# Kernel tuning notes

Measured on AMD Instinct MI355X. Metric: run time of the kernel, lower is better.

The kernel has to match this reference:

```python
import jax, jax.numpy as jnp
import numpy as np

B, D, TOPC = 8, 1024, 256
CIN, DOWN, BR, NR, G = 64, 128, 2, 8, 8
GC = DOWN // G
H = W = 64
LN_EPS = 1e-5


def _ln(x, g, b):
    mu = x.mean(-1, keepdims=True)
    var = ((x - mu) ** 2).mean(-1, keepdims=True)
    return (x - mu) * jax.lax.rsqrt(var + LN_EPS) * g + b


def _gelu(x):
    return jax.nn.gelu(x, approximate=False)


def _sample_topleft(I, IX, IY, IT, x, y):
    # x, y: [B, N] continuous coords; returns [B, CIN, N]
    x = x[:, None, :]
    y = y[:, None, :]
    X = jnp.ceil(x).astype(jnp.int32)
    Y = jnp.ceil(y).astype(jnp.int32)
    z = jnp.zeros_like(X)
    dx = X - x
    dy = Y - y
    b = jnp.arange(B)[:, None, None]
    c = jnp.arange(CIN)[None, :, None]
    wx1 = 0.5 * dx ** 2
    wx2 = dx - wx1
    wy1 = 0.5 * dy ** 2
    wy2 = dy - wy1
    s_a = IT[b, c, X, Y]
    s_e1 = (wy1 * (IX[b, c, X, Y - 1] - 0.5 * I[b, c, X, Y - 1] - 0.5 * I[b, c, z, Y - 1])
            + wy2 * (IX[b, c, X, Y] - 0.5 * I[b, c, X, Y] - 0.5 * I[b, c, z, Y]))
    s_e2 = (wx1 * (IY[b, c, X - 1, Y] - 0.5 * I[b, c, X - 1, Y] - 0.5 * I[b, c, X - 1, z])
            + wx2 * (IY[b, c, X, Y] - 0.5 * I[b, c, X, Y] - 0.5 * I[b, c, X, z]))
    s_c = (wx1 * wy1 * I[b, c, X - 1, Y - 1] + wx2 * wy1 * I[b, c, X, Y - 1]
           + wx1 * wy2 * I[b, c, X - 1, Y] + wx2 * wy2 * I[b, c, X, Y])
    return s_a - s_e1 - s_e2 + s_c


def setup_inputs() -> dict:
    key = jax.random.key(0)
    ks = jax.random.split(key, 20)
    s = 0.02
    return {
        "x": jax.random.normal(ks[0], (B, D, TOPC), jnp.float32),
        "I": jax.random.normal(ks[1], (B, CIN, H, W), jnp.float32),
        "IX": jax.random.normal(ks[2], (B, CIN, H, W), jnp.float32),
        "IY": jax.random.normal(ks[3], (B, CIN, H, W), jnp.float32),
        "IT": jax.random.normal(ks[4], (B, CIN, H, W), jnp.float32),
        "w_idx": jax.random.normal(ks[5], (BR * NR * 4, TOPC), jnp.float32) * s,
        "b_idx": jnp.zeros((BR * NR * 4,), jnp.float32),
        "w_proj": jax.random.normal(ks[6], (DOWN, CIN), jnp.float32) * s,
        "b_proj": jnp.zeros((DOWN,), jnp.float32),
        "w_mask": jax.random.normal(ks[7], (BR * NR * G, TOPC), jnp.float32) * s,
        "b_mask": jnp.zeros((BR * NR * G,), jnp.float32),
        "g1": jnp.ones((DOWN,), jnp.float32),
        "beta1": jnp.zeros((DOWN,), jnp.float32),
        "w_mlp1": jax.random.normal(ks[8], (4 * DOWN, DOWN), jnp.float32) * s,
        "b_mlp1": jnp.zeros((4 * DOWN,), jnp.float32),
        "w_mlp2": jax.random.normal(ks[9], (DOWN, 4 * DOWN), jnp.float32) * s,
        "b_mlp2": jnp.zeros((DOWN,), jnp.float32),
        "g2": jnp.ones((DOWN,), jnp.float32),
        "beta2": jnp.zeros((DOWN,), jnp.float32),
    }


def reference(x, I, IX, IY, IT, w_idx, b_idx, w_proj, b_proj, w_mask, b_mask,
              g1, beta1, w_mlp1, b_mlp1, w_mlp2, b_mlp2, g2, beta2):
    # rect prediction
    p = x @ w_idx.T + b_idx                       # [B, D, BR*NR*4]
    fac = jnp.array([H - 1, W - 1, H - 1, W - 1], jnp.float32)
    p = jax.nn.sigmoid(p.reshape(B, D, BR, NR, 4)) * fac
    p = p.reshape(B, D * BR * NR, 4)
    x1, y1, x2, y2 = p[:, :, 0], p[:, :, 1], p[:, :, 2], p[:, :, 3]
    S = (_sample_topleft(I, IX, IY, IT, x2, y2)
         - _sample_topleft(I, IX, IY, IT, x1, y2)
         - _sample_topleft(I, IX, IY, IT, x2, y1)
         + _sample_topleft(I, IX, IY, IT, x1, y1))  # [B, CIN, N]
    S = S.reshape(B, CIN, D, BR, NR).transpose(0, 2, 3, 4, 1)  # [B, D, BR, NR, CIN]
    rects = _gelu(S @ w_proj.T + b_proj)           # [B, D, BR, NR, DOWN]
    mask = (x @ w_mask.T + b_mask).reshape(B, D * BR, NR, G, 1)
    mask = jax.nn.softmax(mask, axis=2)
    rects = rects.reshape(B, D * BR, NR, G, GC)
    out = (mask * rects).sum(2).reshape(B, D * BR, DOWN)
    out = _ln(out, g1, beta1)
    shortcut = out
    out = _gelu(out @ w_mlp1.T + b_mlp1) @ w_mlp2.T + b_mlp2
    return _ln(out, g2, beta2) + shortcut
```

## Files before the change

kernel.cpp:

```cpp
#include <hip/hip_runtime.h>
#include <hip/hip_bf16.h>
#include <hip/hip_fp16.h>
#include <math.h>

#define BB   8
#define DD   1024

typedef short bh8 __attribute__((ext_vector_type(8)));
typedef float f32x4 __attribute__((ext_vector_type(4)));
typedef _Float16 h2f __attribute__((ext_vector_type(2)));

__device__ __forceinline__ ushort f2bf(float f) {
    uint u = __builtin_bit_cast(uint, f);
    u += 0x7fffu + ((u >> 16) & 1u);
    return (ushort)(u >> 16);
}
__device__ __forceinline__ float asf(uint u)  { return __builtin_bit_cast(float, u); }
__device__ __forceinline__ float bflo(uint u) { return __builtin_bit_cast(float, u << 16); }
__device__ __forceinline__ float bfhi(uint u) { return __builtin_bit_cast(float, u & 0xffff0000u); }
__device__ __forceinline__ uint  pkh(float a, float b) {
    return __builtin_bit_cast(uint, __builtin_amdgcn_cvt_pkrtz(a, b));
}
__device__ __forceinline__ h2f ash2f(uint u) { return __builtin_bit_cast(h2f, u); }

#if __has_builtin(__builtin_amdgcn_fdot2)
__device__ __forceinline__ float fdot2h(h2f a, h2f b, float c) {
    return __builtin_amdgcn_fdot2(a, b, c, false);
}
#else
__device__ __forceinline__ float fdot2h(h2f a, h2f b, float c) {
    return fmaf((float)a.x, (float)b.x, fmaf((float)a.y, (float)b.y, c));
}
#endif

__device__ __forceinline__ uint cvtpk_bf16(float a, float b) {
    uint r;
    asm("v_cvt_pk_bf16_f32 %0, %1, %2" : "=v"(r) : "v"(a), "v"(b));
    return r;
}
__device__ __forceinline__ ushort cvt1_bf16(float a) {
    uint r;
    asm("v_cvt_pk_bf16_f32 %0, %1, %2" : "=v"(r) : "v"(a), "v"(a));
    return (ushort)r;
}

__device__ __forceinline__ float gelu_fast(float x) {
    float x2 = x * x;
#if __has_builtin(__builtin_amdgcn_exp2f)
    float e = __builtin_amdgcn_exp2f(x * fmaf(x2, -0.20588652f, -2.3022082f));
#else
    float e = __expf(-(1.5957691216f * x + 0.14270963f * x * x2));
#endif
    return x * __builtin_amdgcn_rcpf(1.0f + e);
}
__device__ __forceinline__ float sig63(float v) {
    return 63.0f * __builtin_amdgcn_rcpf(1.0f + __expf(-v));
}

__global__ __launch_bounds__(256) void kT_pack(
    const float* __restrict__ w_idx, const float* __restrict__ w_mask,
    const float* __restrict__ w_proj, const float* __restrict__ w1,
    const float* __restrict__ w2,
    ushort* __restrict__ catPh, ushort* __restrict__ catPm,
    ushort* __restrict__ catPl,
    ushort* __restrict__ w_projP, ushort* __restrict__ w1P,
    ushort* __restrict__ w2P)
{
    int bid = blockIdx.x, t = threadIdx.x;
    if (bid < 24) {
        int gid = bid * 256 + t;
        int l = gid & 63, ks = (gid >> 6) & 7, nt = gid >> 9;
        int n = nt * 16 + (l & 15);
        int kbase = ks * 32 + ((l >> 4) << 3);
        const float* src = (n < 64) ? (w_idx + (size_t)n * 256)
                                    : (w_mask + (size_t)(n - 64) * 256);
        ushort* dh = catPh + (size_t)gid * 8;
        ushort* dm = catPm + (size_t)gid * 8;
        ushort* dl = catPl + (size_t)gid * 8;
        #pragma unroll
        for (int j = 0; j < 8; ++j) {
            float v = src[kbase + j];
            ushort h = f2bf(v);
            float hf = __builtin_bit_cast(float, (uint)h << 16);
            float r1 = v - hf;
            ushort m = f2bf(r1); float mf = __builtin_bit_cast(float, (uint)m << 16);
            ushort lo = f2bf(r1 - mf);
            dh[j] = h; dm[j] = m; dl[j] = lo;
        }
    } else if (bid < 28) {
        int g = (bid - 24) * 256 + t;
        int nt = g >> 7, ks = (g >> 6) & 1, l = g & 63;
        int n = nt * 16 + (l & 15), k0 = ks * 32 + (l >> 4) * 8;
        ushort* dst = w_projP + (size_t)g * 8;
        #pragma unroll
        for (int j = 0; j < 8; ++j) dst[j] = f2bf(w_proj[n * 64 + k0 + j]);
    } else if (bid < 60) {
        int g = (bid - 28) * 256 + t;
        int nt = g >> 8, ks = (g >> 6) & 3, l = g & 63;
        int n = nt * 16 + (l & 15), k0 = ks * 32 + (l >> 4) * 8;
        ushort* dst = w1P + (size_t)g * 8;
        #pragma unroll
        for (int j = 0; j < 8; ++j) dst[j] = f2bf(w1[n * 128 + k0 + j]);
    } else {
        int g = (bid - 60) * 256 + t;
        int nt = g >> 10, ks = (g >> 6) & 15, l = g & 63;
        int n = nt * 16 + (l & 15), k0 = ks * 32 + (l >> 4) * 8;
        ushort* dst = w2P + (size_t)g * 8;
        #pragma unroll
        for (int j = 0; j < 8; ++j) dst[j] = f2bf(w2[n * 512 + k0 + j]);
    }
}

__global__ __launch_bounds__(256) void k01(
    const float* __restrict__ x,
    const ushort* __restrict__ catPh, const ushort* __restrict__ catPm,
    const ushort* __restrict__ catPl,
    const float* __restrict__ b_idx, const float* __restrict__ b_mask,
    float* __restrict__ maskw, float* __restrict__ coords,
    const float* __restrict__ I, const float* __restrict__ IX,
    const float* __restrict__ IY, const float* __restrict__ IT,
    uint4* __restrict__ T1, ushort* __restrict__ T2)
{
    __shared__ __align__(16) float sf[6528];
    int t = threadIdx.x;
    int bid = blockIdx.x;

    if (bid >= 2048) {
        float* sOut = sf;
        size_t rowbase = (size_t)(bid - 2048) * 16;
        int w = t >> 6, l = t & 63;

        f32x4 acc[3];
        acc[0] = (f32x4){0.f,0.f,0.f,0.f};
        acc[1] = (f32x4){0.f,0.f,0.f,0.f};
        acc[2] = (f32x4){0.f,0.f,0.f,0.f};
        const float* xr = x + (rowbase + (size_t)(l & 15)) * 256 + ((l >> 4) << 3);

        #pragma unroll
        for (int half = 0; half < 2; ++half) {
            bh8 Ah[4], Am[4], Al[4];
            #pragma unroll
            for (int k4 = 0; k4 < 4; ++k4) {
                int ks = half * 4 + k4;
                float4 v0 = *(const float4*)(xr + ks * 32);
                float4 v1 = *(const float4*)(xr + ks * 32 + 4);
                uint4 uh, um, ul;
                uh.x = cvtpk_bf16(v0.x, v0.y);
                uh.y = cvtpk_bf16(v0.z, v0.w);
                uh.z = cvtpk_bf16(v1.x, v1.y);
                uh.w = cvtpk_bf16(v1.z, v1.w);
                float r0a = v0.x - bflo(uh.x), r0b = v0.y - bfhi(uh.x);
                float r0c = v0.z - bflo(uh.y), r0d = v0.w - bfhi(uh.y);
                float r1a = v1.x - bflo(uh.z), r1b = v1.y - bfhi(uh.z);
                float r1c = v1.z - bflo(uh.w), r1d = v1.w - bfhi(uh.w);
                um.x = cvtpk_bf16(r0a, r0b);
                um.y = cvtpk_bf16(r0c, r0d);
                um.z = cvtpk_bf16(r1a, r1b);
                um.w = cvtpk_bf16(r1c, r1d);
                ul.x = cvtpk_bf16(r0a - bflo(um.x), r0b - bfhi(um.x));
                ul.y = cvtpk_bf16(r0c - bflo(um.y), r0d - bfhi(um.y));
                ul.z = cvtpk_bf16(r1a - bflo(um.z), r1b - bfhi(um.z));
                ul.w = cvtpk_bf16(r1c - bflo(um.w), r1d - bfhi(um.w));
                Ah[k4] = __builtin_bit_cast(bh8, uh);
                Am[k4] = __builtin_bit_cast(bh8, um);
                Al[k4] = __builtin_bit_cast(bh8, ul);
            }
            #pragma unroll
            for (int ntl = 0; ntl < 3; ++ntl) {
                int nt = w * 3 + ntl;
                #pragma unroll
                for (int k4 = 0; k4 < 4; ++k4) {
                    int ks = half * 4 + k4;
                    size_t fo = ((size_t)(nt * 8 + ks) * 64 + l) * 8;
                    bh8 bh = *(const bh8*)(catPh + fo);
                    bh8 bm = *(const bh8*)(catPm + fo);
                    bh8 bl = *(const bh8*)(catPl + fo);
                    acc[ntl] = __builtin_amdgcn_mfma_f32_16x16x32_bf16(Ah[k4], bh, acc[ntl], 0, 0, 0);
                    acc[ntl] = __builtin_amdgcn_mfma_f32_16x16x32_bf16(Ah[k4], bm, acc[ntl], 0, 0, 0);
                    acc[ntl] = __builtin_amdgcn_mfma_f32_16x16x32_bf16(Am[k4], bh, acc[ntl], 0, 0, 0);
                    acc[ntl] = __builtin_amdgcn_mfma_f32_16x16x32_bf16(Ah[k4], bl, acc[ntl], 0, 0, 0);
                    acc[ntl] = __builtin_amdgcn_mfma_f32_16x16x32_bf16(Al[k4], bh, acc[ntl], 0, 0, 0);
                    acc[ntl] = __builtin_amdgcn_mfma_f32_16x16x32_bf16(Am[k4], bm, acc[ntl], 0, 0, 0);
                }
            }
        }
        {
            int r0 = (l >> 4) * 4, cbase = w * 48 + (l & 15);
            #pragma unroll
            for (int ntl = 0; ntl < 3; ++ntl)
                #pragma unroll
                for (int reg = 0; reg < 4; ++reg)
                    sOut[(r0 + reg) * 193 + cbase + ntl * 16] = acc[ntl][reg];
        }
        __syncthreads();

        {
            int row = t >> 4, u = t & 15, br = u >> 3, nr = u & 7;
            const float* so = sOut + row * 193;
            int c0 = br * 32 + nr * 4;
            float4 co;
            co.x = sig63(so[c0 + 0] + b_idx[c0 + 0]);
            co.y = sig63(so[c0 + 1] + b_idx[c0 + 1]);
            co.z = sig63(so[c0 + 2] + b_idx[c0 + 2]);
            co.w = sig63(so[c0 + 3] + b_idx[c0 + 3]);
            *(float4*)(coords + (((rowbase + row) * 16) + (size_t)u) * 4) = co;
        }
        {
            int row = t >> 4, br = (t >> 3) & 1, g = t & 7;
            const float* so = sOut + row * 193 + 64;
            float lg[8];
            float mx = -1e30f;
            #pragma unroll
            for (int nr = 0; nr < 8; ++nr) {
                int idx = br * 64 + nr * 8 + g;
                lg[nr] = so[idx] + b_mask[idx];
                mx = fmaxf(mx, lg[nr]);
            }
            float s = 0.f;
            #pragma unroll
            for (int nr = 0; nr < 8; ++nr) { lg[nr] = __expf(lg[nr] - mx); s += lg[nr]; }
            float inv = __builtin_amdgcn_rcpf(s);
            #pragma unroll
            for (int nr = 0; nr < 8; ++nr)
                maskw[(rowbase + row) * 128 + br * 64 + nr * 8 + g] = lg[nr] * inv;
        }
    } else {
        int chunk = bid & 3, h = (bid >> 2) & 63, b = bid >> 8;
        int hp = h > 0 ? h - 1 : 0;
        int cb = chunk * 16;
        size_t inb  = (size_t)b * 262144 + (size_t)h  * 64;
        size_t inbp = (size_t)b * 262144 + (size_t)hp * 64;

        {
            int c = t >> 4, w4 = (t & 15) << 2;
            size_t o = (size_t)(cb + c) * 4096 + w4;
            int so = c * 68 + w4;
            *(float4*)(sf + 0 * 1088 + so) = *(const float4*)(I  + inb  + o);
            *(float4*)(sf + 1 * 1088 + so) = *(const float4*)(I  + inbp + o);
            *(float4*)(sf + 2 * 1088 + so) = *(const float4*)(IX + inb  + o);
            *(float4*)(sf + 3 * 1088 + so) = *(const float4*)(IY + inb  + o);
            *(float4*)(sf + 4 * 1088 + so) = *(const float4*)(IY + inbp + o);
            *(float4*)(sf + 5 * 1088 + so) = *(const float4*)(IT + inb  + o);
        }
        __syncthreads();

        #pragma unroll
        for (int i = 0; i < 4; ++i) {
            int idx = i * 256 + t; int w = idx >> 4, c = idx & 15;
            int wm = w > 0 ? w - 1 : 0;
            int rb = c * 68;
            float I00 = sf[rb + w],        I0m = sf[rb + wm];
            float Im0 = sf[1088 + rb + w], Imm = sf[1088 + rb + wm];
            float E1  = sf[2176 + rb + w]  - 0.5f * I00;
            float E1m = sf[2176 + rb + wm] - 0.5f * I0m;
            float E2  = sf[3264 + rb + w]  - 0.5f * I00;
            float E2m = sf[4352 + rb + w]  - 0.5f * Im0;
            float v0 = sf[5440 + rb + w];
            float v1 = -E1;
            float v2 = 0.5f * (E1 - E1m);
            float v3 = -E2;
            float v4 = 0.5f * (E2 - E2m);
            float v5 = I00;
            float v6 = 0.5f * (I0m - I00);
            float v7 = 0.5f * (Im0 - I00);
            float v8 = 0.25f * ((Imm - I0m) - (Im0 - I00));
            size_t pt = (((size_t)b * 4096) + (size_t)h * 64 + w) * 64 + (cb + c);
            uint4 o4;
            o4.x = pkh(v0, v1);
            o4.y = pkh(v2, v3);
            o4.z = pkh(v4, v5);
            o4.w = pkh(v6, v7);
            T1[pt] = o4;
            T2[pt] = (ushort)(pkh(v8, 0.f) & 0xffffu);
        }
    }
}

__global__ __launch_bounds__(256) void k2_rects(
    const uint4* __restrict__ T1, const ushort* __restrict__ T2,
    const float* __restrict__ coords,
    const ushort* __restrict__ w_projP, const float* __restrict__ b_proj,
    const float* __restrict__ maskw, const float* __restrict__ g1,
    const float* __restrict__ beta1, float* __restrict__ mid)
{
    __shared__ __align__(16) uint meta_lds[16][32];
    __shared__ __align__(16) float S_lds[16][68];
    __shared__ float mrow[128];
    __shared__ float outr[2][128];
    int bid = blockIdx.x;
    int b = bid & 7, d = bid >> 3;
    int t = threadIdx.x, w = t >> 6, l = t & 63;
    size_t tile = (size_t)b * DD + d;
    if (t < 64) {
        int u = t >> 2, c = t & 3;
        float4 co = *(const float4*)(coords + (tile * 16 + (size_t)u) * 4);
        float x1 = co.x, y1 = co.y, x2 = co.z, y2 = co.w;
        int X1 = (int)ceilf(x1); X1 = X1 < 1 ? 1 : (X1 > 63 ? 63 : X1);
        int X2 = (int)ceilf(x2); X2 = X2 < 1 ? 1 : (X2 > 63 ? 63 : X2);
        int Y1 = (int)ceilf(y1); Y1 = Y1 < 1 ? 1 : (Y1 > 63 ? 63 : Y1);
        int Y2 = (int)ceilf(y2); Y2 = Y2 < 1 ? 1 : (Y2 > 63 ? 63 : Y2);
        float dxa = (float)X1 - x1, dxb = (float)X2 - x2;
        float dya = (float)Y1 - y1, dyb = (float)Y2 - y2;
        int   Xc = (c & 1) ? X1 : X2;
        int   Yc = (c < 2) ? Y2 : Y1;
        float s  = (c == 0 || c == 3) ? 1.f : -1.f;
        float dx = (c & 1) ? dxa : dxb;
        float dy = (c < 2) ? dyb : dya;
        float dx2 = dx * dx, dy2 = dy * dy;
        uint pt = (uint)(Xc * 64 + Yc);
        uint4 wa, wb;
        wa.x = pt * 1024u;
        wa.y = pt * 128u;
        wa.z = pkh(s, s * dy);
        wa.w = pkh(s * dy2, s * dx);
        wb.x = pkh(s * dx2, s * dx * dy);
        wb.y = pkh(s * dx * dy2, s * dx2 * dy);
        wb.z = __builtin_bit_cast(uint, s * dx2 * dy2);
        wb.w = 0u;
        *(uint4*)&meta_lds[u][c * 8 + 0] = wa;
        *(uint4*)&meta_lds[u][c * 8 + 4] = wb;
    }
    if (t >= 128) mrow[t - 128] = maskw[tile * 128 + (t - 128)];

    bh8 bf[2][2];
    #pragma unroll
    for (int ni = 0; ni < 2; ++ni) {
        int nt = w * 2 + ni;
        #pragma unroll
        for (int ks = 0; ks < 2; ++ks)
            bf[ni][ks] = *(const bh8*)(w_projP + ((size_t)(nt * 2 + ks) * 64 + l) * 8);
    }
    __syncthreads();
    const char* t1b = ((const char*)T1) + ((size_t)b << 22) + (size_t)(l * 16);
    const char* t2b = ((const char*)T2) + ((size_t)b << 19) + (size_t)(l * 2);

    int m0 = w * 4;
    uint4 q[2][4]; ushort e8[2][4];
    #pragma unroll
    for (int g = 0; g < 2; ++g) {
        #pragma unroll
        for (int c = 0; c < 4; ++c) {
            uint o1 = __builtin_amdgcn_readfirstlane(meta_lds[m0 + g][c * 8 + 0]);
            uint o2 = __builtin_amdgcn_readfirstlane(meta_lds[m0 + g][c * 8 + 1]);
            q[g][c]  = *(const uint4*)(t1b + o1);
            e8[g][c] = *(const ushort*)(t2b + o2);
        }
    }
    #pragma unroll
    for (int rr = 0; rr < 4; ++rr) {
        int m = m0 + rr;
        int cur = rr & 1;
        uint4 qc[4]; ushort ec[4];
        #pragma unroll
        for (int c = 0; c < 4; ++c) { qc[c] = q[cur][c]; ec[c] = e8[cur][c]; }
        if (rr < 2) {
            int mn = m + 2;
            #pragma unroll
            for (int c = 0; c < 4; ++c) {
                uint o1 = __builtin_amdgcn_readfirstlane(meta_lds[mn][c * 8 + 0]);
                uint o2 = __builtin_amdgcn_readfirstlane(meta_lds[mn][c * 8 + 1]);
                q[cur][c]  = *(const uint4*)(t1b + o1);
                e8[cur][c] = *(const ushort*)(t2b + o2);
            }
        }
        float acc0 = 0.f, acc1 = 0.f;
        #pragma unroll
        for (int c = 0; c < 4; ++c) {
            uint cz = meta_lds[m][c * 8 + 2], cw = meta_lds[m][c * 8 + 3];
            uint bx = meta_lds[m][c * 8 + 4], by = meta_lds[m][c * 8 + 5];
            float bz = asf(meta_lds[m][c * 8 + 6]);
            float ev = __half2float(__builtin_bit_cast(__half, ec[c]));
            float cv = bz * ev;
            cv = fdot2h(ash2f(by), ash2f(qc[c].w), cv);
            cv = fdot2h(ash2f(bx), ash2f(qc[c].z), cv);
            cv = fdot2h(ash2f(cw), ash2f(qc[c].y), cv);
            cv = fdot2h(ash2f(cz), ash2f(qc[c].x), cv);
            if (c & 1) acc1 += cv; else acc0 += cv;
        }
        S_lds[m][l] = acc0 + acc1;
    }
    __syncthreads();

    int am = l & 15, q2 = l >> 4;
    bh8 a0, a1;
    {
        float4 va = *(const float4*)&S_lds[am][q2 * 8];
        float4 vb = *(const float4*)&S_lds[am][q2 * 8 + 4];
        uint4 ua;
        ua.x = cvtpk_bf16(va.x, va.y);
        ua.y = cvtpk_bf16(va.z, va.w);
        ua.z = cvtpk_bf16(vb.x, vb.y);
        ua.w = cvtpk_bf16(vb.z, vb.w);
        a0 = __builtin_bit_cast(bh8, ua);
        float4 vc = *(const float4*)&S_lds[am][32 + q2 * 8];
        float4 vd = *(const float4*)&S_lds[am][32 + q2 * 8 + 4];
        uint4 ub;
        ub.x = cvtpk_bf16(vc.x, vc.y);
        ub.y = cvtpk_bf16(vc.z, vc.w);
        ub.z = cvtpk_bf16(vd.x, vd.y);
        ub.w = cvtpk_bf16(vd.z, vd.w);
        a1 = __builtin_bit_cast(bh8, ub);
    }
    f32x4 cc[2];
    cc[0] = (f32x4){0.f, 0.f, 0.f, 0.f};
    cc[1] = (f32x4){0.f, 0.f, 0.f, 0.f};
    cc[0] = __builtin_amdgcn_mfma_f32_16x16x32_bf16(a0, bf[0][0], cc[0], 0, 0, 0);
    cc[0] = __builtin_amdgcn_mfma_f32_16x16x32_bf16(a1, bf[0][1], cc[0], 0, 0, 0);
    cc[1] = __builtin_amdgcn_mfma_f32_16x16x32_bf16(a0, bf[1][0], cc[1], 0, 0, 0);
    cc[1] = __builtin_amdgcn_mfma_f32_16x16x32_bf16(a1, bf[1][1], cc[1], 0, 0, 0);

    int cl = l & 15;
    #pragma unroll
    for (int ni = 0; ni < 2; ++ni) {
        int nt = w * 2 + ni;
        int col = nt * 16 + cl;
        float bpv = b_proj[col];
        float p = 0.f;
        #pragma unroll
        for (int reg = 0; reg < 4; ++reg) {
            int r = q2 * 4 + reg;
            float v = cc[ni][reg] + bpv;
            p += gelu_fast(v) * mrow[(r >> 3) * 64 + (r & 7) * 8 + nt];
        }
        p += __shfl_xor(p, 16, 64);
        if (q2 == 0) outr[0][col] = p;
        else if (q2 == 2) outr[1][col] = p;
    }
    __syncthreads();

    if (w < 2) {
        float v0 = outr[w][l], v1 = outr[w][l + 64];
        float s = v0 + v1, sq = v0 * v0 + v1 * v1;
        #pragma unroll
        for (int mm = 32; mm > 0; mm >>= 1) {
            s  += __shfl_xor(s, mm, 64);
            sq += __shfl_xor(sq, mm, 64);
        }
        float mu  = s * (1.0f / 128.0f);
        float var = sq * (1.0f / 128.0f) - mu * mu;
        float rs  = rsqrtf(var + 1e-5f);
        size_t ob = (tile * 2 + w) * 128;
        mid[ob + l]      = (v0 - mu) * rs * g1[l]      + beta1[l];
        mid[ob + l + 64] = (v1 - mu) * rs * g1[l + 64] + beta1[l + 64];
    }
}

__global__ __launch_bounds__(256) void k4_mlp(
    const float* __restrict__ mid, const ushort* __restrict__ w1P,
    const float* __restrict__ b1, const ushort* __restrict__ w2P,
    const float* __restrict__ b2, const float* __restrict__ g2,
    const float* __restrict__ beta2, float* __restrict__ outp)
{
    __shared__ float xr[16][132];
    __shared__ __align__(16) ushort Af[4][64][8];
    __shared__ __align__(16) ushort H[16][520];
    __shared__ float oo[16][128];
    __shared__ float b1s[512];
    __shared__ float b2s[128], g2s[128], bt2s[128];
    int t = threadIdx.x, w = t >> 6, l = t & 63;
    int bid = blockIdx.x;
    int mt = (bid & 7) * 128 + (bid >> 3);
    size_t rowbase = (size_t)mt * 16;

    {
        const float4* mg = (const float4*)(mid + rowbase * 128);
        #pragma unroll
        for (int i4 = 0; i4 < 2; ++i4) {
            int i = i4 * 256 + t;
            float4 v = mg[i];
            *(float4*)(&xr[i >> 5][(i & 31) * 4]) = v;
        }
    }
    for (int i = t; i < 512; i += 256) b1s[i] = b1[i];
    if (t < 128) { b2s[t] = b2[t]; g2s[t] = g2[t]; bt2s[t] = beta2[t]; }
    __syncthreads();

    {
        int ks = t >> 6, m = l & 15, c0 = ks * 32 + (l >> 4) * 8;
        uint* dst = (uint*)&Af[ks][l][0];
        #pragma unroll
        for (int j = 0; j < 4; ++j)
            dst[j] = cvtpk_bf16(xr[m][c0 + 2 * j], xr[m][c0 + 2 * j + 1]);
    }
    __syncthreads();

    f32x4 c1[8];
    #pragma unroll
    for (int i = 0; i < 8; ++i) c1[i] = (f32x4){0.f, 0.f, 0.f, 0.f};
    bh8 a[4];
    #pragma unroll
    for (int ks = 0; ks < 4; ++ks) a[ks] = *(const bh8*)&Af[ks][l][0];
    #pragma unroll
    for (int ni = 0; ni < 8; ++ni) {
        int nt = w * 8 + ni;
        #pragma unroll
        for (int ks = 0; ks < 4; ++ks) {
            bh8 bfr = *(const bh8*)(w1P + ((size_t)(nt * 4 + ks) * 64 + l) * 8);
            c1[ni] = __builtin_amdgcn_mfma_f32_16x16x32_bf16(a[ks], bfr, c1[ni], 0, 0, 0);
        }
    }
    #pragma unroll
    for (int ni = 0; ni < 8; ++ni) {
        int nt = w * 8 + ni;
        int col = nt * 16 + (l & 15);
        int r0 = (l >> 4) * 4;
        #pragma unroll
        for (int reg = 0; reg < 4; ++reg)
            H[r0 + reg][col] = cvt1_bf16(gelu_fast(c1[ni][reg] + b1s[col]));
    }
    __syncthreads();

    f32x4 c2[2];
    c2[0] = (f32x4){0.f, 0.f, 0.f, 0.f};
    c2[1] = (f32x4){0.f, 0.f, 0.f, 0.f};
    const char* hb = (const char*)&H[0][0];
    #pragma unroll
    for (int ks2 = 0; ks2 < 16; ++ks2) {
        bh8 af = *(const bh8*)(hb + (l & 15) * 1040 + ks2 * 64 + (l >> 4) * 16);
        #pragma unroll
        for (int i = 0; i < 2; ++i) {
            int nt2 = w * 2 + i;
            bh8 bfr = *(const bh8*)(w2P + ((size_t)(nt2 * 16 + ks2) * 64 + l) * 8);
            c2[i] = __builtin_amdgcn_mfma_f32_16x16x32_bf16(af, bfr, c2[i], 0, 0, 0);
        }
    }
    #pragma unroll
    for (int i = 0; i < 2; ++i) {
        int col = (w * 2 + i) * 16 + (l & 15);
        int r0 = (l >> 4) * 4;
        #pragma unroll
        for (int reg = 0; reg < 4; ++reg) oo[r0 + reg][col] = c2[i][reg] + b2s[col];
    }
    __syncthreads();

    #pragma unroll
    for (int rr = 0; rr < 4; ++rr) {
        int r = w * 4 + rr;
        float v0 = oo[r][l], v1 = oo[r][l + 64];
        float s = v0 + v1, sq = v0 * v0 + v1 * v1;
        #pragma unroll
        for (int m = 32; m > 0; m >>= 1) {
            s  += __shfl_xor(s, m, 64);
            sq += __shfl_xor(sq, m, 64);
        }
        float mu  = s * (1.0f / 128.0f);
        float var = sq * (1.0f / 128.0f) - mu * mu;
        float rs  = rsqrtf(var + 1e-5f);
        size_t ob = (rowbase + r) * 128;
        outp[ob + l]      = (v0 - mu) * rs * g2s[l]      + bt2s[l]      + xr[r][l];
        outp[ob + l + 64] = (v1 - mu) * rs * g2s[l + 64] + bt2s[l + 64] + xr[r][l + 64];
    }
}

extern "C" void kernel_launch(void* const* d_in, const int* in_sizes, int n_in,
                              void* d_out, int out_size, void* d_ws, size_t ws_size,
                              hipStream_t stream) {
    const float* x      = (const float*)d_in[0];
    const float* I      = (const float*)d_in[1];
    const float* IX     = (const float*)d_in[2];
    const float* IY     = (const float*)d_in[3];
    const float* IT     = (const float*)d_in[4];
    const float* w_idx  = (const float*)d_in[5];
    const float* b_idx  = (const float*)d_in[6];
    const float* w_proj = (const float*)d_in[7];
    const float* b_proj = (const float*)d_in[8];
    const float* w_mask = (const float*)d_in[9];
    const float* b_mask = (const float*)d_in[10];
    const float* g1     = (const float*)d_in[11];
    const float* beta1  = (const float*)d_in[12];
    const float* w_mlp1 = (const float*)d_in[13];
    const float* b_mlp1 = (const float*)d_in[14];
    const float* w_mlp2 = (const float*)d_in[15];
    const float* b_mlp2 = (const float*)d_in[16];
    const float* g2     = (const float*)d_in[17];
    const float* beta2  = (const float*)d_in[18];
    float* out = (float*)d_out;

    float* ws = (float*)d_ws;
    ushort* catPh  = (ushort*)ws;
    ushort* catPm  = (ushort*)(ws + 24576);
    ushort* catPl  = (ushort*)(ws + 49152);
    ushort* w_projP = (ushort*)(ws + 73728);
    ushort* w1P     = (ushort*)(ws + 77824);
    ushort* w2P     = (ushort*)(ws + 110592);
    float*  maskw   = ws + 143360;
    float*  coords  = ws + 1191936;
    uint4*  T1      = (uint4*)(ws + 1716224);
    ushort* T2      = (ushort*)(ws + 10104832);

    kT_pack<<<92, 256, 0, stream>>>(w_idx, w_mask, w_proj, w_mlp1, w_mlp2,
                                    catPh, catPm, catPl, w_projP, w1P, w2P);
    k01<<<2560, 256, 0, stream>>>(x, catPh, catPm, catPl, b_idx, b_mask,
                                  maskw, coords, I, IX, IY, IT, T1, T2);
    k2_rects<<<8192, 256, 0, stream>>>(T1, T2, coords, w_projP, b_proj, maskw,
                                       g1, beta1, out);
    k4_mlp<<<1024, 256, 0, stream>>>(out, w1P, b_mlp1, w2P, b_mlp2, g2, beta2, out);
}
```

Baseline: 84.55 us.

## Split coords and texture kernels and skip texture rows no coordinate references

The fused coords/texture kernel is split into two launches. The coords kernel now marks, per batch, which image rows are hit by the ceil of the predicted x-coordinates. The texture kernel then skips building T1/T2 for rows with no flag set, cutting global reads and writes of the integral-image tables. The trade-offs are that the two stages now run serially, with an extra launch and a small flag-clearing block in the pack kernel. The savings also depend on how tightly the coordinates cluster.

```diff
diff --git a/kernel.cpp b/kernel.cpp
--- a/kernel.cpp
+++ b/kernel.cpp
@@ -64,7 +64,7 @@
     ushort* __restrict__ catPh, ushort* __restrict__ catPm,
     ushort* __restrict__ catPl,
     ushort* __restrict__ w_projP, ushort* __restrict__ w1P,
-    ushort* __restrict__ w2P)
+    ushort* __restrict__ w2P, uint* __restrict__ rowflag)
 {
     int bid = blockIdx.x, t = threadIdx.x;
     if (bid < 24) {
@@ -101,178 +101,191 @@
         ushort* dst = w1P + (size_t)g * 8;
         #pragma unroll
         for (int j = 0; j < 8; ++j) dst[j] = f2bf(w1[n * 128 + k0 + j]);
-    } else {
+    } else if (bid < 92) {
         int g = (bid - 60) * 256 + t;
         int nt = g >> 10, ks = (g >> 6) & 15, l = g & 63;
         int n = nt * 16 + (l & 15), k0 = ks * 32 + (l >> 4) * 8;
         ushort* dst = w2P + (size_t)g * 8;
         #pragma unroll
         for (int j = 0; j < 8; ++j) dst[j] = f2bf(w2[n * 512 + k0 + j]);
-    }
-}
-
-__global__ __launch_bounds__(256) void k01(
+    } else {
+        if (t < 128) rowflag[t] = 0u;
+    }
+}
+
+__global__ __launch_bounds__(256) void kA_coords(
     const float* __restrict__ x,
     const ushort* __restrict__ catPh, const ushort* __restrict__ catPm,
     const ushort* __restrict__ catPl,
     const float* __restrict__ b_idx, const float* __restrict__ b_mask,
     float* __restrict__ maskw, float* __restrict__ coords,
+    unsigned char* __restrict__ rowflag)
+{
+    __shared__ __align__(16) float sOut[16 * 193];
+    int t = threadIdx.x;
+    size_t rowbase = (size_t)blockIdx.x * 16;
+    int w = t >> 6, l = t & 63;
+
+    f32x4 acc[3];
+    acc[0] = (f32x4){0.f,0.f,0.f,0.f};
+    acc[1] = (f32x4){0.f,0.f,0.f,0.f};
+    acc[2] = (f32x4){0.f,0.f,0.f,0.f};
+    const float* xr = x + (rowbase + (size_t)(l & 15)) * 256 + ((l >> 4) << 3);
+
+    #pragma unroll
+    for (int half = 0; half < 2; ++half) {
+        bh8 Ah[4], Am[4], Al[4];
+        #pragma unroll
+        for (int k4 = 0; k4 < 4; ++k4) {
+            int ks = half * 4 + k4;
+            float4 v0 = *(const float4*)(xr + ks * 32);
+            float4 v1 = *(const float4*)(xr + ks * 32 + 4);
+            uint4 uh, um, ul;
+            uh.x = cvtpk_bf16(v0.x, v0.y);
+            uh.y = cvtpk_bf16(v0.z, v0.w);
+            uh.z = cvtpk_bf16(v1.x, v1.y);
+            uh.w = cvtpk_bf16(v1.z, v1.w);
+            float r0a = v0.x - bflo(uh.x), r0b = v0.y - bfhi(uh.x);
+            float r0c = v0.z - bflo(uh.y), r0d = v0.w - bfhi(uh.y);
+            float r1a = v1.x - bflo(uh.z), r1b = v1.y - bfhi(uh.z);
+            float r1c = v1.z - bflo(uh.w), r1d = v1.w - bfhi(uh.w);
+            um.x = cvtpk_bf16(r0a, r0b);
+            um.y = cvtpk_bf16(r0c, r0d);
+            um.z = cvtpk_bf16(r1a, r1b);
+            um.w = cvtpk_bf16(r1c, r1d);
+            ul.x = cvtpk_bf16(r0a - bflo(um.x), r0b - bfhi(um.x));
+            ul.y = cvtpk_bf16(r0c - bflo(um.y), r0d - bfhi(um.y));
+            ul.z = cvtpk_bf16(r1a - bflo(um.z), r1b - bfhi(um.z));
+            ul.w = cvtpk_bf16(r1c - bflo(um.w), r1d - bfhi(um.w));
+            Ah[k4] = __builtin_bit_cast(bh8, uh);
+            Am[k4] = __builtin_bit_cast(bh8, um);
+            Al[k4] = __builtin_bit_cast(bh8, ul);
+        }
+        #pragma unroll
+        for (int ntl = 0; ntl < 3; ++ntl) {
+            int nt = w * 3 + ntl;
+            #pragma unroll
+            for (int k4 = 0; k4 < 4; ++k4) {
+                int ks = half * 4 + k4;
+                size_t fo = ((size_t)(nt * 8 + ks) * 64 + l) * 8;
+                bh8 bh = *(const bh8*)(catPh + fo);
+                bh8 bm = *(const bh8*)(catPm + fo);
+                bh8 bl = *(const bh8*)(catPl + fo);
+                acc[ntl] = __builtin_amdgcn_mfma_f32_16x16x32_bf16(Ah[k4], bh, acc[ntl], 0, 0, 0);
+                acc[ntl] = __builtin_amdgcn_mfma_f32_16x16x32_bf16(Ah[k4], bm, acc[ntl], 0, 0, 0);
+                acc[ntl] = __builtin_amdgcn_mfma_f32_16x16x32_bf16(Am[k4], bh, acc[ntl], 0, 0, 0);
+                acc[ntl] = __builtin_amdgcn_mfma_f32_16x16x32_bf16(Ah[k4], bl, acc[ntl], 0, 0, 0);
+                acc[ntl] = __builtin_amdgcn_mfma_f32_16x16x32_bf16(Al[k4], bh, acc[ntl], 0, 0, 0);
+                acc[ntl] = __builtin_amdgcn_mfma_f32_16x16x32_bf16(Am[k4], bm, acc[ntl], 0, 0, 0);
+            }
+        }
+    }
+    {
+        int r0 = (l >> 4) * 4, cbase = w * 48 + (l & 15);
+        #pragma unroll
+        for (int ntl = 0; ntl < 3; ++ntl)
+            #pragma unroll
+            for (int reg = 0; reg < 4; ++reg)
+                sOut[(r0 + reg) * 193 + cbase + ntl * 16] = acc[ntl][reg];
+    }
+    __syncthreads();
+
+    {
+        int row = t >> 4, u = t & 15, br = u >> 3, nr = u & 7;
+        const float* so = sOut + row * 193;
+        int c0 = br * 32 + nr * 4;
+        float4 co;
+        co.x = sig63(so[c0 + 0] + b_idx[c0 + 0]);
+        co.y = sig63(so[c0 + 1] + b_idx[c0 + 1]);
+        co.z = sig63(so[c0 + 2] + b_idx[c0 + 2]);
+        co.w = sig63(so[c0 + 3] + b_idx[c0 + 3]);
+        size_t tile = rowbase + row;
+        *(float4*)(coords + (tile * 16 + (size_t)u) * 4) = co;
+        int bb = (int)(tile >> 10);
+        int Xa = (int)ceilf(co.x); Xa = Xa < 1 ? 1 : (Xa > 63 ? 63 : Xa);
+        int Xb = (int)ceilf(co.z); Xb = Xb < 1 ? 1 : (Xb > 63 ? 63 : Xb);
+        rowflag[bb * 64 + Xa] = 1;
+        rowflag[bb * 64 + Xb] = 1;
+    }
+    {
+        int row = t >> 4, br = (t >> 3) & 1, g = t & 7;
+        const float* so = sOut + row * 193 + 64;
+        float lg[8];
+        float mx = -1e30f;
+        #pragma unroll
+        for (int nr = 0; nr < 8; ++nr) {
+            int idx = br * 64 + nr * 8 + g;
+            lg[nr] = so[idx] + b_mask[idx];
+            mx = fmaxf(mx, lg[nr]);
+        }
+        float s = 0.f;
+        #pragma unroll
+        for (int nr = 0; nr < 8; ++nr) { lg[nr] = __expf(lg[nr] - mx); s += lg[nr]; }
+        float inv = __builtin_amdgcn_rcpf(s);
+        #pragma unroll
+        for (int nr = 0; nr < 8; ++nr)
+            maskw[(rowbase + row) * 128 + br * 64 + nr * 8 + g] = lg[nr] * inv;
+    }
+}
+
+__global__ __launch_bounds__(256) void kB_tex(
     const float* __restrict__ I, const float* __restrict__ IX,
     const float* __restrict__ IY, const float* __restrict__ IT,
+    const unsigned char* __restrict__ rowflag,
     uint4* __restrict__ T1, ushort* __restrict__ T2)
 {
     __shared__ __align__(16) float sf[6528];
     int t = threadIdx.x;
     int bid = blockIdx.x;
-
-    if (bid >= 2048) {
-        float* sOut = sf;
-        size_t rowbase = (size_t)(bid - 2048) * 16;
-        int w = t >> 6, l = t & 63;
-
-        f32x4 acc[3];
-        acc[0] = (f32x4){0.f,0.f,0.f,0.f};
-        acc[1] = (f32x4){0.f,0.f,0.f,0.f};
-        acc[2] = (f32x4){0.f,0.f,0.f,0.f};
-        const float* xr = x + (rowbase + (size_t)(l & 15)) * 256 + ((l >> 4) << 3);
-
-        #pragma unroll
-        for (int half = 0; half < 2; ++half) {
-            bh8 Ah[4], Am[4], Al[4];
-            #pragma unroll
-            for (int k4 = 0; k4 < 4; ++k4) {
-                int ks = half * 4 + k4;
-                float4 v0 = *(const float4*)(xr + ks * 32);
-                float4 v1 = *(const float4*)(xr + ks * 32 + 4);
-                uint4 uh, um, ul;
-                uh.x = cvtpk_bf16(v0.x, v0.y);
-                uh.y = cvtpk_bf16(v0.z, v0.w);
-                uh.z = cvtpk_bf16(v1.x, v1.y);
-                uh.w = cvtpk_bf16(v1.z, v1.w);
-                float r0a = v0.x - bflo(uh.x), r0b = v0.y - bfhi(uh.x);
-                float r0c = v0.z - bflo(uh.y), r0d = v0.w - bfhi(uh.y);
-                float r1a = v1.x - bflo(uh.z), r1b = v1.y - bfhi(uh.z);
-                float r1c = v1.z - bflo(uh.w), r1d = v1.w - bfhi(uh.w);
-                um.x = cvtpk_bf16(r0a, r0b);
-                um.y = cvtpk_bf16(r0c, r0d);
-                um.z = cvtpk_bf16(r1a, r1b);
-                um.w = cvtpk_bf16(r1c, r1d);
-                ul.x = cvtpk_bf16(r0a - bflo(um.x), r0b - bfhi(um.x));
-                ul.y = cvtpk_bf16(r0c - bflo(um.y), r0d - bfhi(um.y));
-                ul.z = cvtpk_bf16(r1a - bflo(um.z), r1b - bfhi(um.z));
-                ul.w = cvtpk_bf16(r1c - bflo(um.w), r1d - bfhi(um.w));
-                Ah[k4] = __builtin_bit_cast(bh8, uh);
-                Am[k4] = __builtin_bit_cast(bh8, um);
-                Al[k4] = __builtin_bit_cast(bh8, ul);
-            }
-            #pragma unroll
-            for (int ntl = 0; ntl < 3; ++ntl) {
-                int nt = w * 3 + ntl;
-                #pragma unroll
-                for (int k4 = 0; k4 < 4; ++k4) {
-                    int ks = half * 4 + k4;
-                    size_t fo = ((size_t)(nt * 8 + ks) * 64 + l) * 8;
-                    bh8 bh = *(const bh8*)(catPh + fo);
-                    bh8 bm = *(const bh8*)(catPm + fo);
-                    bh8 bl = *(const bh8*)(catPl + fo);
-                    acc[ntl] = __builtin_amdgcn_mfma_f32_16x16x32_bf16(Ah[k4], bh, acc[ntl], 0, 0, 0);
-                    acc[ntl] = __builtin_amdgcn_mfma_f32_16x16x32_bf16(Ah[k4], bm, acc[ntl], 0, 0, 0);
-                    acc[ntl] = __builtin_amdgcn_mfma_f32_16x16x32_bf16(Am[k4], bh, acc[ntl], 0, 0, 0);
-                    acc[ntl] = __builtin_amdgcn_mfma_f32_16x16x32_bf16(Ah[k4], bl, acc[ntl], 0, 0, 0);
-                    acc[ntl] = __builtin_amdgcn_mfma_f32_16x16x32_bf16(Al[k4], bh, acc[ntl], 0, 0, 0);
-                    acc[ntl] = __builtin_amdgcn_mfma_f32_16x16x32_bf16(Am[k4], bm, acc[ntl], 0, 0, 0);
-                }
-            }
-        }
-        {
-            int r0 = (l >> 4) * 4, cbase = w * 48 + (l & 15);
-            #pragma unroll
-            for (int ntl = 0; ntl < 3; ++ntl)
-                #pragma unroll
-                for (int reg = 0; reg < 4; ++reg)
-                    sOut[(r0 + reg) * 193 + cbase + ntl * 16] = acc[ntl][reg];
-        }
-        __syncthreads();
-
-        {
-            int row = t >> 4, u = t & 15, br = u >> 3, nr = u & 7;
-            const float* so = sOut + row * 193;
-            int c0 = br * 32 + nr * 4;
-            float4 co;
-            co.x = sig63(so[c0 + 0] + b_idx[c0 + 0]);
-            co.y = sig63(so[c0 + 1] + b_idx[c0 + 1]);
-            co.z = sig63(so[c0 + 2] + b_idx[c0 + 2]);
-            co.w = sig63(so[c0 + 3] + b_idx[c0 + 3]);
-            *(float4*)(coords + (((rowbase + row) * 16) + (size_t)u) * 4) = co;
-        }
-        {
-            int row = t >> 4, br = (t >> 3) & 1, g = t & 7;
-            const float* so = sOut + row * 193 + 64;
-            float lg[8];
-            float mx = -1e30f;
-            #pragma unroll
-            for (int nr = 0; nr < 8; ++nr) {
-                int idx = br * 64 + nr * 8 + g;
-                lg[nr] = so[idx] + b_mask[idx];
-                mx = fmaxf(mx, lg[nr]);
-            }
-            float s = 0.f;
-            #pragma unroll
-            for (int nr = 0; nr < 8; ++nr) { lg[nr] = __expf(lg[nr] - mx); s += lg[nr]; }
-            float inv = __builtin_amdgcn_rcpf(s);
-            #pragma unroll
-            for (int nr = 0; nr < 8; ++nr)
-                maskw[(rowbase + row) * 128 + br * 64 + nr * 8 + g] = lg[nr] * inv;
-        }
-    } else {
-        int chunk = bid & 3, h = (bid >> 2) & 63, b = bid >> 8;
-        int hp = h > 0 ? h - 1 : 0;
-        int cb = chunk * 16;
-        size_t inb  = (size_t)b * 262144 + (size_t)h  * 64;
-        size_t inbp = (size_t)b * 262144 + (size_t)hp * 64;
-
-        {
-            int c = t >> 4, w4 = (t & 15) << 2;
-            size_t o = (size_t)(cb + c) * 4096 + w4;
-            int so = c * 68 + w4;
-            *(float4*)(sf + 0 * 1088 + so) = *(const float4*)(I  + inb  + o);
-            *(float4*)(sf + 1 * 1088 + so) = *(const float4*)(I  + inbp + o);
-            *(float4*)(sf + 2 * 1088 + so) = *(const float4*)(IX + inb  + o);
-            *(float4*)(sf + 3 * 1088 + so) = *(const float4*)(IY + inb  + o);
-            *(float4*)(sf + 4 * 1088 + so) = *(const float4*)(IY + inbp + o);
-            *(float4*)(sf + 5 * 1088 + so) = *(const float4*)(IT + inb  + o);
-        }
-        __syncthreads();
-
-        #pragma unroll
-        for (int i = 0; i < 4; ++i) {
-            int idx = i * 256 + t; int w = idx >> 4, c = idx & 15;
-            int wm = w > 0 ? w - 1 : 0;
-            int rb = c * 68;
-            float I00 = sf[rb + w],        I0m = sf[rb + wm];
-            float Im0 = sf[1088 + rb + w], Imm = sf[1088 + rb + wm];
-            float E1  = sf[2176 + rb + w]  - 0.5f * I00;
-            float E1m = sf[2176 + rb + wm] - 0.5f * I0m;
-            float E2  = sf[3264 + rb + w]  - 0.5f * I00;
-            float E2m = sf[4352 + rb + w]  - 0.5f * Im0;
-            float v0 = sf[5440 + rb + w];
-            float v1 = -E1;
-            float v2 = 0.5f * (E1 - E1m);
-            float v3 = -E2;
-            float v4 = 0.5f * (E2 - E2m);
-            float v5 = I00;
-            float v6 = 0.5f * (I0m - I00);
-            float v7 = 0.5f * (Im0 - I00);
-            float v8 = 0.25f * ((Imm - I0m) - (Im0 - I00));
-            size_t pt = (((size_t)b * 4096) + (size_t)h * 64 + w) * 64 + (cb + c);
-            uint4 o4;
-            o4.x = pkh(v0, v1);
-            o4.y = pkh(v2, v3);
-            o4.z = pkh(v4, v5);
-            o4.w = pkh(v6, v7);
-            T1[pt] = o4;
-            T2[pt] = (ushort)(pkh(v8, 0.f) & 0xffffu);
-        }
+    int chunk = bid & 3, h = (bid >> 2) & 63, b = bid >> 8;
+    if (rowflag[b * 64 + h] == 0) return;
+
+    int hp = h > 0 ? h - 1 : 0;
+    int cb = chunk * 16;
+    size_t inb  = (size_t)b * 262144 + (size_t)h  * 64;
+    size_t inbp = (size_t)b * 262144 + (size_t)hp * 64;
+
+    {
+        int c = t >> 4, w4 = (t & 15) << 2;
+        size_t o = (size_t)(cb + c) * 4096 + w4;
+        int so = c * 68 + w4;
+        *(float4*)(sf + 0 * 1088 + so) = *(const float4*)(I  + inb  + o);
+        *(float4*)(sf + 1 * 1088 + so) = *(const float4*)(I  + inbp + o);
+        *(float4*)(sf + 2 * 1088 + so) = *(const float4*)(IX + inb  + o);
+        *(float4*)(sf + 3 * 1088 + so) = *(const float4*)(IY + inb  + o);
+        *(float4*)(sf + 4 * 1088 + so) = *(const float4*)(IY + inbp + o);
+        *(float4*)(sf + 5 * 1088 + so) = *(const float4*)(IT + inb  + o);
+    }
+    __syncthreads();
+
+    #pragma unroll
+    for (int i = 0; i < 4; ++i) {
+        int idx = i * 256 + t; int w = idx >> 4, c = idx & 15;
+        int wm = w > 0 ? w - 1 : 0;
+        int rb = c * 68;
+        float I00 = sf[rb + w],        I0m = sf[rb + wm];
+        float Im0 = sf[1088 + rb + w], Imm = sf[1088 + rb + wm];
+        float E1  = sf[2176 + rb + w]  - 0.5f * I00;
+        float E1m = sf[2176 + rb + wm] - 0.5f * I0m;
+        float E2  = sf[3264 + rb + w]  - 0.5f * I00;
+        float E2m = sf[4352 + rb + w]  - 0.5f * Im0;
+        float v0 = sf[5440 + rb + w];
+        float v1 = -E1;
+        float v2 = 0.5f * (E1 - E1m);
+        float v3 = -E2;
+        float v4 = 0.5f * (E2 - E2m);
+        float v5 = I00;
+        float v6 = 0.5f * (I0m - I00);
+        float v7 = 0.5f * (Im0 - I00);
+        float v8 = 0.25f * ((Imm - I0m) - (Im0 - I00));
+        size_t pt = (((size_t)b * 4096) + (size_t)h * 64 + w) * 64 + (cb + c);
+        uint4 o4;
+        o4.x = pkh(v0, v1);
+        o4.y = pkh(v2, v3);
+        o4.z = pkh(v4, v5);
+        o4.w = pkh(v6, v7);
+        T1[pt] = o4;
+        T2[pt] = (ushort)(pkh(v8, 0.f) & 0xffffu);
     }
 }
 
@@ -587,11 +600,14 @@
     float*  coords  = ws + 1191936;
     uint4*  T1      = (uint4*)(ws + 1716224);
     ushort* T2      = (ushort*)(ws + 10104832);
-
-    kT_pack<<<92, 256, 0, stream>>>(w_idx, w_mask, w_proj, w_mlp1, w_mlp2,
-                                    catPh, catPm, catPl, w_projP, w1P, w2P);
-    k01<<<2560, 256, 0, stream>>>(x, catPh, catPm, catPl, b_idx, b_mask,
-                                  maskw, coords, I, IX, IY, IT, T1, T2);
+    unsigned char* rowflag = (unsigned char*)(ws + 11153408);
+
+    kT_pack<<<93, 256, 0, stream>>>(w_idx, w_mask, w_proj, w_mlp1, w_mlp2,
+                                    catPh, catPm, catPl, w_projP, w1P, w2P,
+                                    (uint*)rowflag);
+    kA_coords<<<512, 256, 0, stream>>>(x, catPh, catPm, catPl, b_idx, b_mask,
+                                       maskw, coords, rowflag);
+    kB_tex<<<2048, 256, 0, stream>>>(I, IX, IY, IT, rowflag, T1, T2);
     k2_rects<<<8192, 256, 0, stream>>>(T1, T2, coords, w_projP, b_proj, maskw,
                                        g1, beta1, out);
     k4_mlp<<<1024, 256, 0, stream>>>(out, w1P, b_mlp1, w2P, b_mlp2, g2, beta2, out);
```

After: 81.41 us. 1.04x faster.
